# Optimization experiments

Measured on AMD Instinct MI355X. Metric: run time of the kernel, lower is better.

Reference implementation:

```python
import jax, jax.numpy as jnp
import numpy as np

N = 100_000      # nodes
E = 3_200_000    # edges (avg degree 32)
F_IN, H1, H2, C = 1433, 200, 80, 7


def setup_inputs() -> dict:
    key = jax.random.key(0)
    ks = jax.random.split(key, 10)
    x = jax.random.normal(ks[0], (N, F_IN), jnp.float32)
    edge_src = jax.random.randint(ks[1], (E,), 0, N)
    edge_dst = jax.random.randint(ks[2], (E,), 0, N)
    edge_w = jax.random.uniform(ks[3], (E,), jnp.float32)
    # GraphConvolution.reset_parameters: uniform(-1/sqrt(out), 1/sqrt(out))
    s1 = 1.0 / np.sqrt(H1).astype(np.float32)
    W1 = jax.random.uniform(ks[4], (F_IN, H1), jnp.float32, -s1, s1)
    b1 = jax.random.uniform(ks[5], (H1,), jnp.float32, -s1, s1)
    s2 = 1.0 / np.sqrt(H2).astype(np.float32)
    W2 = jax.random.uniform(ks[6], (H1, H2), jnp.float32, -s2, s2)
    b2 = jax.random.uniform(ks[7], (H2,), jnp.float32, -s2, s2)
    # nn.Linear(80, 7)
    sf = 1.0 / np.sqrt(H2).astype(np.float32)
    Wfc = jax.random.uniform(ks[8], (H2, C), jnp.float32, -sf, sf)
    bfc = jax.random.uniform(ks[9], (C,), jnp.float32, -sf, sf)
    return {"x": x, "edge_src": edge_src, "edge_dst": edge_dst, "edge_w": edge_w,
            "W1": W1, "b1": b1, "W2": W2, "b2": b2, "Wfc": Wfc, "bfc": bfc}


def reference(x, edge_src, edge_dst, edge_w, W1, b1, W2, b2, Wfc, bfc):
    n = x.shape[0]

    def spmm(h):  # out[dst] += w * h[src]  == torch.spmm(adj, h)
        return jax.ops.segment_sum(edge_w[:, None] * h[edge_src], edge_dst,
                                   num_segments=n)

    h = jax.nn.relu(spmm(x @ W1) + b1)   # GraphConvolution 1 + ReLU (dropout: eval)
    h = jax.nn.relu(spmm(h @ W2) + b2)   # GraphConvolution 2 + ReLU
    return h @ Wfc + bfc                  # fc_1: [N, 7] logits
```

## Files before the change

kernel.cpp:

```cpp
#include <hip/hip_runtime.h>

#define F_IN 1433
#define H1 200
#define H2 80
#define NC 7

typedef __bf16 bf16x8 __attribute__((ext_vector_type(8)));
typedef float f32x4 __attribute__((ext_vector_type(4)));

__device__ __forceinline__ unsigned short bf16_bits(__bf16 h) {
    union { __bf16 h; unsigned short u; } c; c.h = h; return c.u;
}
__device__ __forceinline__ void split_bf16(float a, __bf16& hi, __bf16& lo) {
    hi = (__bf16)a;
    lo = (__bf16)(a - (float)hi);
}

struct AF { float v[8]; };

__device__ __forceinline__ void glds16(const void* g, void* l) {
    __builtin_amdgcn_global_load_lds(
        (const __attribute__((address_space(1))) unsigned int*)g,
        (__attribute__((address_space(3))) unsigned int*)l, 16, 0, 0);
}

template <int K, int KSTEPS, int COLS, int WR, int WC, int MT, int NT, bool BIAS>
__global__ __launch_bounds__(256, 4)
void gemm_mfma_bstage(const float* __restrict__ A, const unsigned short* __restrict__ Bpre,
                      const float* __restrict__ bias, float* __restrict__ C,
                      int M, int NREAL) {
    static_assert(WR * WC == 4, "4 waves");
    static_assert(WR * MT * 16 == 64, "rows");
    static_assert(WC * NT * 16 == COLS, "cols");
    constexpr int THREADS = 256;
    constexpr int PER_STEP = 2 * 4 * COLS * 8;
    constexpr int CH = COLS * 8;
    constexpr bool PART = (KSTEPS * 32 > K);

    __shared__ alignas(16) unsigned short Bs[PER_STEP];

    const int tid = threadIdx.x;
    const int wave = tid >> 6, lane = tid & 63;
    const int l15 = lane & 15, l4 = lane >> 4;
    const int wr = wave / WC, wc = wave % WC;
    const int row0 = blockIdx.x * 64 + wr * (MT * 16);
    const int colbase = wc * (NT * 16);

    f32x4 acc[MT][NT];
    #pragma unroll
    for (int m = 0; m < MT; ++m)
        #pragma unroll
        for (int n = 0; n < NT; ++n) acc[m][n] = (f32x4){0.f, 0.f, 0.f, 0.f};

    const float* arow[MT];
    #pragma unroll
    for (int m = 0; m < MT; ++m) {
        int r = row0 + m * 16 + l15;
        if (r >= M) r = M - 1;
        arow[m] = A + (size_t)r * K;
    }

    auto loadA = [&](int s, AF* dst) {
        const int kb = s * 32 + l4 * 8;
        #pragma unroll
        for (int m = 0; m < MT; ++m) {
            const float* ap = arow[m] + kb;
            if (PART && s == KSTEPS - 1) {
                #pragma unroll
                for (int j = 0; j < 8; ++j) dst[m].v[j] = (kb + j < K) ? ap[j] : 0.f;
            } else {
                #pragma unroll
                for (int j = 0; j < 8; ++j) dst[m].v[j] = ap[j];
            }
        }
    };

    auto stageB = [&](int s) {
        const unsigned short* src = Bpre + (size_t)s * PER_STEP;
        #pragma unroll 4
        for (int c = tid; c < CH; c += THREADS)
            glds16(src + (size_t)c * 8, &Bs[c * 8]);
    };

    AF aCur[MT], aNxt[MT];
    loadA(0, aCur);
    stageB(0);

    for (int s = 0; s < KSTEPS; ++s) {
        __syncthreads();
        bf16x8 aHi[MT], aLo[MT];
        #pragma unroll
        for (int m = 0; m < MT; ++m)
            #pragma unroll
            for (int j = 0; j < 8; ++j) {
                __bf16 hi, lo;
                split_bf16(aCur[m].v[j], hi, lo);
                aHi[m][j] = hi;
                aLo[m][j] = lo;
            }
        if (s + 1 < KSTEPS) loadA(s + 1, aNxt);

        #pragma unroll
        for (int n = 0; n < NT; ++n) {
            const int colb = colbase + n * 16 + l15;
            bf16x8 bHi = *(const bf16x8*)&Bs[((0 + l4) * COLS + colb) * 8];
            bf16x8 bLo = *(const bf16x8*)&Bs[((4 + l4) * COLS + colb) * 8];
            #pragma unroll
            for (int m = 0; m < MT; ++m) {
                acc[m][n] = __builtin_amdgcn_mfma_f32_16x16x32_bf16(aHi[m], bHi, acc[m][n], 0, 0, 0);
                acc[m][n] = __builtin_amdgcn_mfma_f32_16x16x32_bf16(aLo[m], bHi, acc[m][n], 0, 0, 0);
                acc[m][n] = __builtin_amdgcn_mfma_f32_16x16x32_bf16(aHi[m], bLo, acc[m][n], 0, 0, 0);
            }
        }
        __syncthreads();
        if (s + 1 < KSTEPS) stageB(s + 1);
        #pragma unroll
        for (int m = 0; m < MT; ++m) aCur[m] = aNxt[m];
    }

    #pragma unroll
    for (int m = 0; m < MT; ++m) {
        const int rbase = row0 + m * 16 + l4 * 4;
        #pragma unroll
        for (int n = 0; n < NT; ++n) {
            int col = colbase + n * 16 + l15;
            if (col >= NREAL) continue;
            float bv = BIAS ? bias[col] : 0.f;
            #pragma unroll
            for (int r = 0; r < 4; ++r) {
                int gr = rbase + r;
                if (gr < M) C[(size_t)gr * NREAL + col] = acc[m][n][r] + bv;
            }
        }
    }
}

__global__ void convert_B(const float* __restrict__ W, unsigned short* __restrict__ out,
                          int K, int NREAL, int KSTEPS, int COLS) {
    const int per = 2 * 4 * COLS * 8;
    long long total = (long long)KSTEPS * per;
    long long i = (long long)blockIdx.x * blockDim.x + threadIdx.x;
    long long stride = (long long)gridDim.x * blockDim.x;
    for (; i < total; i += stride) {
        int s = (int)(i / per);
        int r = (int)(i % per);
        int hl = r / (4 * COLS * 8); r %= 4 * COLS * 8;
        int k8 = r / (COLS * 8);     r %= COLS * 8;
        int col = r >> 3, j = r & 7;
        int k = s * 32 + k8 * 8 + j;
        float v = (k < K && col < NREAL) ? W[(size_t)k * NREAL + col] : 0.f;
        __bf16 hi, lo;
        split_bf16(v, hi, lo);
        out[i] = bf16_bits(hl ? lo : hi);
    }
}

__global__ void gemm_tiled(const float* __restrict__ A, const float* __restrict__ B,
                           const float* __restrict__ bias, float* __restrict__ C,
                           int M, int K, int N, int tilesN) {
    const int bx = blockIdx.x % tilesN;
    const int by = blockIdx.x / tilesN;
    const int tid = threadIdx.x;
    const int tx = tid & 15, ty = tid >> 4;
    __shared__ float Asf[64][17];
    __shared__ float Bsf[16][65];
    float acc[4][4] = {};
    const int row0 = by * 64, col0 = bx * 64;
    for (int k0 = 0; k0 < K; k0 += 16) {
        #pragma unroll
        for (int l = 0; l < 4; ++l) {
            int e = tid + l * 256;
            int r = e >> 4, kk = e & 15;
            int gr = row0 + r, gk = k0 + kk;
            Asf[r][kk] = (gr < M && gk < K) ? A[(size_t)gr * K + gk] : 0.f;
        }
        #pragma unroll
        for (int l = 0; l < 4; ++l) {
            int e = tid + l * 256;
            int kk = e >> 6, c = e & 63;
            int gk = k0 + kk, gc = col0 + c;
            Bsf[kk][c] = (gk < K && gc < N) ? B[(size_t)gk * N + gc] : 0.f;
        }
        __syncthreads();
        #pragma unroll
        for (int kk = 0; kk < 16; ++kk) {
            float a[4], b[4];
            #pragma unroll
            for (int i = 0; i < 4; ++i) a[i] = Asf[ty + 16 * i][kk];
            #pragma unroll
            for (int j = 0; j < 4; ++j) b[j] = Bsf[kk][tx + 16 * j];
            #pragma unroll
            for (int i = 0; i < 4; ++i)
                #pragma unroll
                for (int j = 0; j < 4; ++j) acc[i][j] += a[i] * b[j];
        }
        __syncthreads();
    }
    #pragma unroll
    for (int i = 0; i < 4; ++i) {
        int gr = row0 + ty + 16 * i;
        if (gr >= M) continue;
        #pragma unroll
        for (int j = 0; j < 4; ++j) {
            int gc = col0 + tx + 16 * j;
            if (gc >= N) continue;
            float v = acc[i][j];
            if (bias) v += bias[gc];
            C[(size_t)gr * N + gc] = v;
        }
    }
}

__global__ void zero_ints(int* __restrict__ p, int n) {
    int i = blockIdx.x * blockDim.x + threadIdx.x;
    int stride = gridDim.x * blockDim.x;
    for (; i < n; i += stride) p[i] = 0;
}

__global__ void hist_dst(const int* __restrict__ dst, int* __restrict__ counts, int E) {
    int i = blockIdx.x * blockDim.x + threadIdx.x;
    int stride = gridDim.x * blockDim.x;
    for (; i < E; i += stride) atomicAdd(&counts[dst[i]], 1);
}

__global__ void chunk_sums(const int* __restrict__ counts, int* __restrict__ csum, int N) {
    __shared__ int s[256];
    int b = blockIdx.x, t = threadIdx.x;
    int base = b * 2048 + t * 8;
    int loc = 0;
    #pragma unroll
    for (int i = 0; i < 8; ++i) {
        int gi = base + i;
        if (gi < N) loc += counts[gi];
    }
    s[t] = loc;
    __syncthreads();
    for (int off = 128; off > 0; off >>= 1) {
        if (t < off) s[t] += s[t + off];
        __syncthreads();
    }
    if (t == 0) csum[b] = s[0];
}

__global__ void scan_chunks(const int* __restrict__ csum, int* __restrict__ cbase, int NB) {
    if (blockIdx.x == 0 && threadIdx.x == 0) {
        int run = 0;
        for (int b = 0; b < NB; ++b) { cbase[b] = run; run += csum[b]; }
    }
}

__global__ void scan_final(const int* __restrict__ counts, const int* __restrict__ cbase,
                           int* __restrict__ row_start, int* __restrict__ cursor, int N) {
    __shared__ int s[256];
    int b = blockIdx.x, t = threadIdx.x;
    int base = b * 2048 + t * 8;
    int loc = 0;
    #pragma unroll
    for (int i = 0; i < 8; ++i) {
        int gi = base + i;
        if (gi < N) loc += counts[gi];
    }
    s[t] = loc;
    __syncthreads();
    for (int off = 1; off < 256; off <<= 1) {
        int v = (t >= off) ? s[t - off] : 0;
        __syncthreads();
        s[t] += v;
        __syncthreads();
    }
    int run = cbase[b] + s[t] - loc;
    for (int i = 0; i < 8; ++i) {
        int gi = base + i;
        if (gi < N) {
            row_start[gi] = run;
            cursor[gi] = run;
            run += counts[gi];
        }
    }
}

__global__ void scatter_edges(const int* __restrict__ src, const int* __restrict__ dst,
                              const float* __restrict__ w, int* __restrict__ cursor,
                              int2* __restrict__ csr, int E) {
    int i = blockIdx.x * blockDim.x + threadIdx.x;
    int stride = gridDim.x * blockDim.x;
    for (; i < E; i += stride) {
        int d = dst[i];
        int pos = atomicAdd(&cursor[d], 1);
        csr[pos] = make_int2(src[i], __float_as_int(w[i]));
    }
}

template <int D, bool RELU>
__global__ __launch_bounds__(256)
void spmm_csr(const float* __restrict__ h, const int2* __restrict__ csr,
              const int* __restrict__ row_start, const int* __restrict__ counts,
              const float* __restrict__ bias, float* __restrict__ out, int N) {
    constexpr int VF = D / 4;
    constexpr int G = 256 / VF;
    const int g = threadIdx.x / VF;
    const int slot = threadIdx.x - g * VF;
    if (g >= G) return;
    const int row = blockIdx.x * G + g;
    if (row >= N) return;

    const int p = row_start[row], len = counts[row];
    f32x4 acc = ((const f32x4*)bias)[slot];

    int2 e0 = make_int2(0, 0), e1 = e0, e2 = e0, e3 = e0;
    if (len > 0) e0 = csr[p];
    if (len > 1) e1 = csr[p + 1];
    if (len > 2) e2 = csr[p + 2];
    if (len > 3) e3 = csr[p + 3];

    for (int q = 0; q < len; q += 4) {
        const int2 c0 = e0, c1 = e1, c2 = e2, c3 = e3;
        const int rem = len - q;
        if (q + 4 < len) e0 = csr[p + q + 4];
        if (q + 5 < len) e1 = csr[p + q + 5];
        if (q + 6 < len) e2 = csr[p + q + 6];
        if (q + 7 < len) e3 = csr[p + q + 7];
        f32x4 h0 = ((const f32x4*)(h + (size_t)c0.x * D))[slot];
        acc += h0 * __int_as_float(c0.y);
        if (rem > 1) {
            f32x4 h1 = ((const f32x4*)(h + (size_t)c1.x * D))[slot];
            acc += h1 * __int_as_float(c1.y);
        }
        if (rem > 2) {
            f32x4 h2 = ((const f32x4*)(h + (size_t)c2.x * D))[slot];
            acc += h2 * __int_as_float(c2.y);
        }
        if (rem > 3) {
            f32x4 h3 = ((const f32x4*)(h + (size_t)c3.x * D))[slot];
            acc += h3 * __int_as_float(c3.y);
        }
    }
    if (RELU) {
        #pragma unroll
        for (int c = 0; c < 4; ++c) acc[c] = acc[c] > 0.f ? acc[c] : 0.f;
    }
    ((f32x4*)(out + (size_t)row * D))[slot] = acc;
}

template <int D, int NCOL>
__global__ __launch_bounds__(256)
void spmm_fc(const float* __restrict__ h, const int2* __restrict__ csr,
             const int* __restrict__ row_start, const int* __restrict__ counts,
             const float* __restrict__ bias, const float* __restrict__ Wfc,
             const float* __restrict__ bfc, float* __restrict__ out, int N) {
    constexpr int VF = D / 4;
    constexpr int G = 256 / VF;
    __shared__ float sh[G][D];
    __shared__ float sW[D * NCOL];
    __shared__ float sb[NCOL];
    for (int i = threadIdx.x; i < D * NCOL; i += 256) sW[i] = Wfc[i];
    if (threadIdx.x < NCOL) sb[threadIdx.x] = bfc[threadIdx.x];

    const int g = threadIdx.x / VF;
    const int slot = threadIdx.x - g * VF;
    const int row = blockIdx.x * G + g;
    const bool active = (g < G) && (row < N);

    if (active) {
        const int p = row_start[row], len = counts[row];
        f32x4 acc = ((const f32x4*)bias)[slot];
        int2 e0 = make_int2(0, 0), e1 = e0, e2 = e0, e3 = e0;
        if (len > 0) e0 = csr[p];
        if (len > 1) e1 = csr[p + 1];
        if (len > 2) e2 = csr[p + 2];
        if (len > 3) e3 = csr[p + 3];
        for (int q = 0; q < len; q += 4) {
            const int2 c0 = e0, c1 = e1, c2 = e2, c3 = e3;
            const int rem = len - q;
            if (q + 4 < len) e0 = csr[p + q + 4];
            if (q + 5 < len) e1 = csr[p + q + 5];
            if (q + 6 < len) e2 = csr[p + q + 6];
            if (q + 7 < len) e3 = csr[p + q + 7];
            f32x4 h0 = ((const f32x4*)(h + (size_t)c0.x * D))[slot];
            acc += h0 * __int_as_float(c0.y);
            if (rem > 1) {
                f32x4 h1 = ((const f32x4*)(h + (size_t)c1.x * D))[slot];
                acc += h1 * __int_as_float(c1.y);
            }
            if (rem > 2) {
                f32x4 h2 = ((const f32x4*)(h + (size_t)c2.x * D))[slot];
                acc += h2 * __int_as_float(c2.y);
            }
            if (rem > 3) {
                f32x4 h3 = ((const f32x4*)(h + (size_t)c3.x * D))[slot];
                acc += h3 * __int_as_float(c3.y);
            }
        }
        #pragma unroll
        for (int c = 0; c < 4; ++c) acc[c] = acc[c] > 0.f ? acc[c] : 0.f;
        ((f32x4*)&sh[g][0])[slot] = acc;
    }
    __syncthreads();

    const int idx = threadIdx.x;
    if (idx < G * NCOL) {
        const int gr = idx / NCOL, c = idx - gr * NCOL;
        const int orow = blockIdx.x * G + gr;
        if (orow < N) {
            float s = sb[c];
            #pragma unroll 8
            for (int j = 0; j < D; ++j) s += sh[gr][j] * sW[j * NCOL + c];
            out[(size_t)orow * NCOL + c] = s;
        }
    }
}

__global__ void init_bias_kernel(float* __restrict__ agg, const float* __restrict__ bias,
                                 long long n, int D) {
    long long i = (long long)blockIdx.x * blockDim.x + threadIdx.x;
    long long stride = (long long)gridDim.x * blockDim.x;
    for (; i < n; i += stride) agg[i] = bias[(int)(i % D)];
}

template <int D>
__global__ void spmm_edges(const float* __restrict__ h, const int* __restrict__ src,
                           const int* __restrict__ dst, const float* __restrict__ w,
                           float* __restrict__ agg, int E) {
    int e = blockIdx.x * 4 + (threadIdx.x >> 6);
    int lane = threadIdx.x & 63;
    if (e >= E) return;
    int s = src[e], d = dst[e];
    float wt = w[e];
    const float* hs = h + (size_t)s * D;
    float* ad = agg + (size_t)d * D;
    for (int j = lane; j < D; j += 64) atomicAdd(&ad[j], wt * hs[j]);
}

__global__ void relu_kernel(float* __restrict__ x, long long n) {
    long long i = (long long)blockIdx.x * blockDim.x + threadIdx.x;
    long long stride = (long long)gridDim.x * blockDim.x;
    for (; i < n; i += stride) {
        float v = x[i];
        x[i] = v > 0.f ? v : 0.f;
    }
}

extern "C" void kernel_launch(void* const* d_in, const int* in_sizes, int n_in,
                              void* d_out, int out_size, void* d_ws, size_t ws_size,
                              hipStream_t stream) {
    const float* x        = (const float*)d_in[0];
    const int*   edge_src = (const int*)d_in[1];
    const int*   edge_dst = (const int*)d_in[2];
    const float* edge_w   = (const float*)d_in[3];
    const float* W1       = (const float*)d_in[4];
    const float* b1       = (const float*)d_in[5];
    const float* W2       = (const float*)d_in[6];
    const float* b2       = (const float*)d_in[7];
    const float* Wfc      = (const float*)d_in[8];
    const float* bfc      = (const float*)d_in[9];
    float* out = (float*)d_out;

    const int N = in_sizes[0] / F_IN;
    const int E = in_sizes[1];
    const int NB = (N + 2047) / 2048;

    float* h0  = (float*)d_ws;
    float* agg = h0 + (size_t)N * H1;
    int* counts    = (int*)(agg + (size_t)N * H1);
    int* row_start = counts + N;
    int* cursor    = row_start + N;
    int* csum      = cursor + N;
    int* cbase     = csum + NB;
    size_t csr_off = (size_t)(cbase + NB) - (size_t)d_ws;
    csr_off = (csr_off + 15) & ~(size_t)15;
    int2* csr = (int2*)((char*)d_ws + csr_off);
    size_t boff = csr_off + (size_t)E * sizeof(int2);
    boff = (boff + 15) & ~(size_t)15;
    const size_t B1n = 45ull * 2 * 4 * 224 * 8;
    const size_t B2n = 7ull * 2 * 4 * 80 * 8;
    unsigned short* B1p = (unsigned short*)((char*)d_ws + boff);
    unsigned short* B2p = B1p + B1n;
    size_t needed = boff + (B1n + B2n) * sizeof(unsigned short);

    float* h1 = agg;
    float* h2 = h0;

    const int MB = (N + 63) / 64;

    if (ws_size >= needed) {
        convert_B<<<(int)((B1n + 255) / 256), 256, 0, stream>>>(W1, B1p, F_IN, H1, 45, 224);
        convert_B<<<(int)((B2n + 255) / 256), 256, 0, stream>>>(W2, B2p, H1, H2, 7, 80);

        zero_ints<<<256, 256, 0, stream>>>(counts, N);
        hist_dst<<<2048, 256, 0, stream>>>(edge_dst, counts, E);
        chunk_sums<<<NB, 256, 0, stream>>>(counts, csum, N);
        scan_chunks<<<1, 64, 0, stream>>>(csum, cbase, NB);
        scan_final<<<NB, 256, 0, stream>>>(counts, cbase, row_start, cursor, N);
        scatter_edges<<<2048, 256, 0, stream>>>(edge_src, edge_dst, edge_w, cursor, csr, E);

        gemm_mfma_bstage<F_IN, 45, 224, 2, 2, 2, 7, false><<<MB, 256, 0, stream>>>(x, B1p, nullptr, h0, N, H1);
        {
            constexpr int G1 = 256 / (H1 / 4);
            spmm_csr<H1, true><<<(N + G1 - 1) / G1, 256, 0, stream>>>(h0, csr, row_start, counts, b1, h1, N);
        }

        gemm_mfma_bstage<H1, 7, 80, 4, 1, 1, 5, false><<<MB, 256, 0, stream>>>(h1, B2p, nullptr, h2, N, H2);

        {
            constexpr int G2 = 256 / (H2 / 4);
            spmm_fc<H2, NC><<<(N + G2 - 1) / G2, 256, 0, stream>>>(h2, csr, row_start, counts, b2, Wfc, bfc, out, N);
        }
    } else {
        const int tilesM = (N + 63) / 64;
        gemm_tiled<<<tilesM * 4, 256, 0, stream>>>(x, W1, nullptr, h0, N, F_IN, H1, 4);
        init_bias_kernel<<<2048, 256, 0, stream>>>(agg, b1, (long long)N * H1, H1);
        spmm_edges<H1><<<(E + 3) / 4, 256, 0, stream>>>(h0, edge_src, edge_dst, edge_w, agg, E);
        relu_kernel<<<2048, 256, 0, stream>>>(agg, (long long)N * H1);
        gemm_tiled<<<tilesM * 2, 256, 0, stream>>>(h1, W2, nullptr, h2, N, H1, H2, 2);
        init_bias_kernel<<<2048, 256, 0, stream>>>(agg, b2, (long long)N * H2, H2);
        spmm_edges<H2><<<(E + 3) / 4, 256, 0, stream>>>(h2, edge_src, edge_dst, edge_w, agg, E);
        relu_kernel<<<2048, 256, 0, stream>>>(agg, (long long)N * H2);
        gemm_tiled<<<tilesM, 256, 0, stream>>>(agg, Wfc, bfc, out, N, H2, NC, 1);
    }
}
```

Before: 1.266 ms.

## Double-buffer GEMM B stage with 512-thread blocks; nontemporal CSR loads in SpMM

The MFMA GEMM now uses two LDS buffers for B, so the next k-step's B tile is issued before the current step's MFMAs. That removes one barrier per iteration and lets the B transfer overlap compute. Blocks grow to 512 threads covering 128 rows, so each staged B tile is reused across more rows, at the cost of twice the LDS and larger blocks that may lower occupancy. The SpMM kernels also switch CSR edge reads and the output store to nontemporal loads and stores, to reduce cache pollution by streamed data.

```diff
diff --git a/kernel.cpp b/kernel.cpp
--- a/kernel.cpp
+++ b/kernel.cpp
@@ -7,6 +7,7 @@
 
 typedef __bf16 bf16x8 __attribute__((ext_vector_type(8)));
 typedef float f32x4 __attribute__((ext_vector_type(4)));
+typedef int i32x2 __attribute__((ext_vector_type(2)));
 
 __device__ __forceinline__ unsigned short bf16_bits(__bf16 h) {
     union { __bf16 h; unsigned short u; } c; c.h = h; return c.u;
@@ -25,25 +26,25 @@
 }
 
 template <int K, int KSTEPS, int COLS, int WR, int WC, int MT, int NT, bool BIAS>
-__global__ __launch_bounds__(256, 4)
-void gemm_mfma_bstage(const float* __restrict__ A, const unsigned short* __restrict__ Bpre,
-                      const float* __restrict__ bias, float* __restrict__ C,
-                      int M, int NREAL) {
-    static_assert(WR * WC == 4, "4 waves");
-    static_assert(WR * MT * 16 == 64, "rows");
+__global__ __launch_bounds__(512, 4)
+void gemm_mfma_dbuf(const float* __restrict__ A, const unsigned short* __restrict__ Bpre,
+                    const float* __restrict__ bias, float* __restrict__ C,
+                    int M, int NREAL) {
+    static_assert(WR * WC == 8, "8 waves");
+    static_assert(WR * MT * 16 == 128, "rows");
     static_assert(WC * NT * 16 == COLS, "cols");
-    constexpr int THREADS = 256;
+    constexpr int THREADS = 512;
     constexpr int PER_STEP = 2 * 4 * COLS * 8;
     constexpr int CH = COLS * 8;
     constexpr bool PART = (KSTEPS * 32 > K);
 
-    __shared__ alignas(16) unsigned short Bs[PER_STEP];
+    __shared__ alignas(16) unsigned short Bs[2][PER_STEP];
 
     const int tid = threadIdx.x;
     const int wave = tid >> 6, lane = tid & 63;
     const int l15 = lane & 15, l4 = lane >> 4;
     const int wr = wave / WC, wc = wave % WC;
-    const int row0 = blockIdx.x * 64 + wr * (MT * 16);
+    const int row0 = blockIdx.x * 128 + wr * (MT * 16);
     const int colbase = wc * (NT * 16);
 
     f32x4 acc[MT][NT];
@@ -75,19 +76,20 @@
         }
     };
 
-    auto stageB = [&](int s) {
+    auto stageB = [&](int s, int b) {
         const unsigned short* src = Bpre + (size_t)s * PER_STEP;
-        #pragma unroll 4
         for (int c = tid; c < CH; c += THREADS)
-            glds16(src + (size_t)c * 8, &Bs[c * 8]);
+            glds16(src + (size_t)c * 8, &Bs[b][c * 8]);
     };
 
     AF aCur[MT], aNxt[MT];
+    stageB(0, 0);
     loadA(0, aCur);
-    stageB(0);
-
+    __syncthreads();
+
+    int cb = 0;
     for (int s = 0; s < KSTEPS; ++s) {
-        __syncthreads();
+        if (s + 1 < KSTEPS) stageB(s + 1, cb ^ 1);
         bf16x8 aHi[MT], aLo[MT];
         #pragma unroll
         for (int m = 0; m < MT; ++m)
@@ -100,11 +102,12 @@
             }
         if (s + 1 < KSTEPS) loadA(s + 1, aNxt);
 
+        const unsigned short* bsc = &Bs[cb][0];
         #pragma unroll
         for (int n = 0; n < NT; ++n) {
             const int colb = colbase + n * 16 + l15;
-            bf16x8 bHi = *(const bf16x8*)&Bs[((0 + l4) * COLS + colb) * 8];
-            bf16x8 bLo = *(const bf16x8*)&Bs[((4 + l4) * COLS + colb) * 8];
+            bf16x8 bHi = *(const bf16x8*)&bsc[((0 + l4) * COLS + colb) * 8];
+            bf16x8 bLo = *(const bf16x8*)&bsc[((4 + l4) * COLS + colb) * 8];
             #pragma unroll
             for (int m = 0; m < MT; ++m) {
                 acc[m][n] = __builtin_amdgcn_mfma_f32_16x16x32_bf16(aHi[m], bHi, acc[m][n], 0, 0, 0);
@@ -113,7 +116,7 @@
             }
         }
         __syncthreads();
-        if (s + 1 < KSTEPS) stageB(s + 1);
+        cb ^= 1;
         #pragma unroll
         for (int m = 0; m < MT; ++m) aCur[m] = aNxt[m];
     }
@@ -293,7 +296,7 @@
 
 template <int D, bool RELU>
 __global__ __launch_bounds__(256)
-void spmm_csr(const float* __restrict__ h, const int2* __restrict__ csr,
+void spmm_csr(const float* __restrict__ h, const i32x2* __restrict__ csr,
               const int* __restrict__ row_start, const int* __restrict__ counts,
               const float* __restrict__ bias, float* __restrict__ out, int N) {
     constexpr int VF = D / 4;
@@ -307,19 +310,19 @@
     const int p = row_start[row], len = counts[row];
     f32x4 acc = ((const f32x4*)bias)[slot];
 
-    int2 e0 = make_int2(0, 0), e1 = e0, e2 = e0, e3 = e0;
-    if (len > 0) e0 = csr[p];
-    if (len > 1) e1 = csr[p + 1];
-    if (len > 2) e2 = csr[p + 2];
-    if (len > 3) e3 = csr[p + 3];
+    i32x2 e0 = (i32x2){0, 0}, e1 = e0, e2 = e0, e3 = e0;
+    if (len > 0) e0 = __builtin_nontemporal_load(&csr[p]);
+    if (len > 1) e1 = __builtin_nontemporal_load(&csr[p + 1]);
+    if (len > 2) e2 = __builtin_nontemporal_load(&csr[p + 2]);
+    if (len > 3) e3 = __builtin_nontemporal_load(&csr[p + 3]);
 
     for (int q = 0; q < len; q += 4) {
-        const int2 c0 = e0, c1 = e1, c2 = e2, c3 = e3;
+        const i32x2 c0 = e0, c1 = e1, c2 = e2, c3 = e3;
         const int rem = len - q;
-        if (q + 4 < len) e0 = csr[p + q + 4];
-        if (q + 5 < len) e1 = csr[p + q + 5];
-        if (q + 6 < len) e2 = csr[p + q + 6];
-        if (q + 7 < len) e3 = csr[p + q + 7];
+        if (q + 4 < len) e0 = __builtin_nontemporal_load(&csr[p + q + 4]);
+        if (q + 5 < len) e1 = __builtin_nontemporal_load(&csr[p + q + 5]);
+        if (q + 6 < len) e2 = __builtin_nontemporal_load(&csr[p + q + 6]);
+        if (q + 7 < len) e3 = __builtin_nontemporal_load(&csr[p + q + 7]);
         f32x4 h0 = ((const f32x4*)(h + (size_t)c0.x * D))[slot];
         acc += h0 * __int_as_float(c0.y);
         if (rem > 1) {
@@ -339,12 +342,12 @@
         #pragma unroll
         for (int c = 0; c < 4; ++c) acc[c] = acc[c] > 0.f ? acc[c] : 0.f;
     }
-    ((f32x4*)(out + (size_t)row * D))[slot] = acc;
+    __builtin_nontemporal_store(acc, (f32x4*)(out + (size_t)row * D) + slot);
 }
 
 template <int D, int NCOL>
 __global__ __launch_bounds__(256)
-void spmm_fc(const float* __restrict__ h, const int2* __restrict__ csr,
+void spmm_fc(const float* __restrict__ h, const i32x2* __restrict__ csr,
              const int* __restrict__ row_start, const int* __restrict__ counts,
              const float* __restrict__ bias, const float* __restrict__ Wfc,
              const float* __restrict__ bfc, float* __restrict__ out, int N) {
@@ -364,18 +367,18 @@
     if (active) {
         const int p = row_start[row], len = counts[row];
         f32x4 acc = ((const f32x4*)bias)[slot];
-        int2 e0 = make_int2(0, 0), e1 = e0, e2 = e0, e3 = e0;
-        if (len > 0) e0 = csr[p];
-        if (len > 1) e1 = csr[p + 1];
-        if (len > 2) e2 = csr[p + 2];
-        if (len > 3) e3 = csr[p + 3];
+        i32x2 e0 = (i32x2){0, 0}, e1 = e0, e2 = e0, e3 = e0;
+        if (len > 0) e0 = __builtin_nontemporal_load(&csr[p]);
+        if (len > 1) e1 = __builtin_nontemporal_load(&csr[p + 1]);
+        if (len > 2) e2 = __builtin_nontemporal_load(&csr[p + 2]);
+        if (len > 3) e3 = __builtin_nontemporal_load(&csr[p + 3]);
         for (int q = 0; q < len; q += 4) {
-            const int2 c0 = e0, c1 = e1, c2 = e2, c3 = e3;
+            const i32x2 c0 = e0, c1 = e1, c2 = e2, c3 = e3;
             const int rem = len - q;
-            if (q + 4 < len) e0 = csr[p + q + 4];
-            if (q + 5 < len) e1 = csr[p + q + 5];
-            if (q + 6 < len) e2 = csr[p + q + 6];
-            if (q + 7 < len) e3 = csr[p + q + 7];
+            if (q + 4 < len) e0 = __builtin_nontemporal_load(&csr[p + q + 4]);
+            if (q + 5 < len) e1 = __builtin_nontemporal_load(&csr[p + q + 5]);
+            if (q + 6 < len) e2 = __builtin_nontemporal_load(&csr[p + q + 6]);
+            if (q + 7 < len) e3 = __builtin_nontemporal_load(&csr[p + q + 7]);
             f32x4 h0 = ((const f32x4*)(h + (size_t)c0.x * D))[slot];
             acc += h0 * __int_as_float(c0.y);
             if (rem > 1) {
@@ -480,7 +483,7 @@
     float* h1 = agg;
     float* h2 = h0;
 
-    const int MB = (N + 63) / 64;
+    const int MB = (N + 127) / 128;
 
     if (ws_size >= needed) {
         convert_B<<<(int)((B1n + 255) / 256), 256, 0, stream>>>(W1, B1p, F_IN, H1, 45, 224);
@@ -493,17 +496,17 @@
         scan_final<<<NB, 256, 0, stream>>>(counts, cbase, row_start, cursor, N);
         scatter_edges<<<2048, 256, 0, stream>>>(edge_src, edge_dst, edge_w, cursor, csr, E);
 
-        gemm_mfma_bstage<F_IN, 45, 224, 2, 2, 2, 7, false><<<MB, 256, 0, stream>>>(x, B1p, nullptr, h0, N, H1);
+        gemm_mfma_dbuf<F_IN, 45, 224, 4, 2, 2, 7, false><<<MB, 512, 0, stream>>>(x, B1p, nullptr, h0, N, H1);
         {
             constexpr int G1 = 256 / (H1 / 4);
-            spmm_csr<H1, true><<<(N + G1 - 1) / G1, 256, 0, stream>>>(h0, csr, row_start, counts, b1, h1, N);
-        }
-
-        gemm_mfma_bstage<H1, 7, 80, 4, 1, 1, 5, false><<<MB, 256, 0, stream>>>(h1, B2p, nullptr, h2, N, H2);
+            spmm_csr<H1, true><<<(N + G1 - 1) / G1, 256, 0, stream>>>(h0, (const i32x2*)csr, row_start, counts, b1, h1, N);
+        }
+
+        gemm_mfma_dbuf<H1, 7, 80, 8, 1, 1, 5, false><<<MB, 512, 0, stream>>>(h1, B2p, nullptr, h2, N, H2);
 
         {
             constexpr int G2 = 256 / (H2 / 4);
-            spmm_fc<H2, NC><<<(N + G2 - 1) / G2, 256, 0, stream>>>(h2, csr, row_start, counts, b2, Wfc, bfc, out, N);
+            spmm_fc<H2, NC><<<(N + G2 - 1) / G2, 256, 0, stream>>>(h2, (const i32x2*)csr, row_start, counts, b2, Wfc, bfc, out, N);
         }
     } else {
         const int tilesM = (N + 63) / 64;
```

After: 1.337 ms. +5.6%, slower.
